# Kernel tuning notes

Hardware: AMD Instinct MI355X
Metric: run time of the kernel (lower is better)

Reference implementation:

```python
import jax, jax.numpy as jnp
import numpy as np

B, H, W, C = 4096, 64, 64, 8


def setup_inputs() -> dict:
    key = jax.random.key(0)
    k1, _ = jax.random.split(key)
    x = jax.random.randint(k1, (B, H, W, C), 0, 2).astype(jnp.float32)
    opp_start = jnp.array([3.0, 6.0], dtype=jnp.float32)
    return {"x": x, "opp_start": opp_start}


def reference(x, opp_start):
    Bb, Hh, Ww, _ = x.shape
    HW = Hh * Ww
    food = (x[..., 1] == 1.0)          # [B,H,W] bool
    opp = (x[..., 3] == 1.0)           # [B,H,W] bool
    food_f = food.reshape(Bb, HW)
    opp_f = opp.reshape(Bb, HW)
    n_food = food_f.sum(-1)
    n_opp = opp_f.sum(-1)

    # first opponent index in row-major order (torch.nonzero ordering)
    first_opp = jnp.argmax(opp_f, axis=-1)            # [B]
    orow = (first_opp // Ww).astype(jnp.float32)
    ocol = (first_opp % Ww).astype(jnp.float32)

    rows = jnp.arange(Hh, dtype=jnp.float32)[:, None]   # [H,1]
    cols = jnp.arange(Ww, dtype=jnp.float32)[None, :]   # [1,W]
    d = jnp.sqrt((rows - orow[:, None, None]) ** 2 + (cols - ocol[:, None, None]) ** 2)  # [B,H,W]
    INF = jnp.float32(np.inf)
    d = jnp.where(food, d, INF).reshape(Bb, HW)        # dists only at food cells

    min_idx = jnp.argmin(d, axis=-1)                   # first min, row-major (matches torch)
    min1 = jnp.take_along_axis(d, min_idx[:, None], axis=-1)[:, 0]
    d2 = d.at[jnp.arange(Bb), min_idx].set(INF)
    min2 = d2.min(-1)
    diff = min2 - min1                                 # sorted_dists[1]-sorted_dists[0]

    matches_start = (orow == opp_start[0]) & (ocol == opp_start[1])
    branchA = (n_food > 1) & (n_opp > 0) & (~matches_start)
    ambiguous = (branchA & (diff < 0.1)) | ((n_food > 1) & (~branchA))
    pick_nearest = (branchA & (diff >= 0.1)) | (n_food == 1)

    onehot_near = jax.nn.one_hot(min_idx, HW, dtype=jnp.float32)  # [B,HW]
    hit = jnp.where(ambiguous[:, None], food_f.astype(jnp.float32),
                    jnp.where(pick_nearest[:, None], onehot_near, 0.0))
    g_logits = -10.0 + 20.0 * hit
    return g_logits.reshape(Bb, Hh, Ww)
```

## Files before the change

### kernel.cpp

```cpp
#include <hip/hip_runtime.h>
#include <math.h>

constexpr int HWPIX = 4096;
constexpr int BLK   = 256;

__global__ __launch_bounds__(BLK) void oracle_kernel(
    const float* __restrict__ x,
    const float* __restrict__ opp_start,
    float* __restrict__ out)
{
    const int b    = blockIdx.x;
    const int t    = threadIdx.x;
    const int lane = t & 63;
    const int wv   = t >> 6;

    const float4* xb = (const float4*)(x + (size_t)b * HWPIX * 8);

    __shared__ unsigned char s_food[HWPIX];
    __shared__ int   s_stat[4][3];
    __shared__ float s_m1[4], s_m2[4];
    __shared__ int   s_i1[4];
    __shared__ int   s_hdr[3];
    __shared__ int   s_dec[3];

    const bool even  = (t & 1) == 0;
    const int  pbase = t >> 1;
    const int  j0    = b & 31;
    int fc = 0, oc = 0, fo = HWPIX;

    #pragma unroll
    for (int jo = 0; jo < 32; jo += 8) {
        float4 v[8];
        int    jj[8];
        #pragma unroll
        for (int ji = 0; ji < 8; ++ji) {
            jj[ji] = (j0 + jo + ji) & 31;
            v[ji]  = xb[t + BLK * jj[ji]];
        }
        #pragma unroll
        for (int ji = 0; ji < 8; ++ji) {
            const int  p    = pbase + 128 * jj[ji];
            const bool food = (v[ji].y == 1.0f);
            const bool opp  = (v[ji].w == 1.0f);
            if (even) {
                s_food[p] = food ? 1 : 0;
                fc += food ? 1 : 0;
                oc += opp  ? 1 : 0;
                fo  = opp ? min(fo, p) : fo;
            }
        }
    }

    #pragma unroll
    for (int off = 32; off > 0; off >>= 1) {
        fc += __shfl_down(fc, off);
        oc += __shfl_down(oc, off);
        fo  = min(fo, __shfl_down(fo, off));
    }
    if (lane == 0) { s_stat[wv][0] = fc; s_stat[wv][1] = oc; s_stat[wv][2] = fo; }
    __syncthreads();
    if (t == 0) {
        int nf = 0, no = 0, f = HWPIX;
        for (int w = 0; w < 4; ++w) {
            nf += s_stat[w][0]; no += s_stat[w][1]; f = min(f, s_stat[w][2]);
        }
        if (f == HWPIX) f = 0;
        s_hdr[0] = nf; s_hdr[1] = no; s_hdr[2] = f;
    }
    __syncthreads();
    const int n_food    = s_hdr[0];
    const int n_opp     = s_hdr[1];
    const int first_opp = s_hdr[2];
    const float orow = (float)(first_opp >> 6);
    const float ocol = (float)(first_opp & 63);

    float m1 = INFINITY, m2 = INFINITY;
    int   i1 = 0x7fffffff;
    #pragma unroll
    for (int k = 0; k < 16; ++k) {
        const int p = t + BLK * k;
        if (s_food[p]) {
            const float dr = (float)(p >> 6) - orow;
            const float dc = (float)(p & 63) - ocol;
            const float d  = sqrtf(dr * dr + dc * dc);
            if (d < m1)      { m2 = m1; m1 = d; i1 = p; }
            else if (d < m2) { m2 = d; }
        }
    }
    #pragma unroll
    for (int off = 32; off > 0; off >>= 1) {
        const float n1 = __shfl_down(m1, off);
        const int   j1 = __shfl_down(i1, off);
        const float n2 = __shfl_down(m2, off);
        if (n1 < m1 || (n1 == m1 && j1 < i1)) {
            m2 = fminf(m1, n2); m1 = n1; i1 = j1;
        } else {
            m2 = fminf(m2, n1);
        }
    }
    if (lane == 0) { s_m1[wv] = m1; s_m2[wv] = m2; s_i1[wv] = i1; }
    __syncthreads();

    if (t == 0) {
        m1 = s_m1[0]; m2 = s_m2[0]; i1 = s_i1[0];
        for (int w = 1; w < 4; ++w) {
            const float n1 = s_m1[w], n2 = s_m2[w];
            const int   j1 = s_i1[w];
            if (n1 < m1 || (n1 == m1 && j1 < i1)) {
                m2 = fminf(m1, n2); m1 = n1; i1 = j1;
            } else {
                m2 = fminf(m2, n1);
            }
        }
        const float diff = m2 - m1;
        const bool matches_start = (orow == opp_start[0]) && (ocol == opp_start[1]);
        const bool branchA   = (n_food > 1) && (n_opp > 0) && !matches_start;
        const bool ambiguous = (branchA && (diff < 0.1f)) || ((n_food > 1) && !branchA);
        const bool pick      = (branchA && (diff >= 0.1f)) || (n_food == 1);
        s_dec[0] = ambiguous ? 1 : 0;
        s_dec[1] = pick ? 1 : 0;
        s_dec[2] = i1;
    }
    __syncthreads();

    const int amb = s_dec[0], pick = s_dec[1], midx = s_dec[2];
    const unsigned* s_food32 = (const unsigned*)s_food;
    float4* ob4 = (float4*)(out + (size_t)b * HWPIX);
    #pragma unroll
    for (int k = 0; k < 4; ++k) {
        const int kk = (k + b) & 3;
        const int q = t + BLK * kk;
        const unsigned fm = s_food32[q];
        float4 r;
        float* rp = &r.x;
        #pragma unroll
        for (int i = 0; i < 4; ++i) {
            const int p = 4 * q + i;
            const bool f = (fm >> (8 * i)) & 0xFF;
            const float hit = amb ? (f ? 1.0f : 0.0f)
                                  : (pick ? ((p == midx) ? 1.0f : 0.0f) : 0.0f);
            rp[i] = -10.0f + 20.0f * hit;
        }
        ob4[q] = r;
    }
}

extern "C" void kernel_launch(void* const* d_in, const int* in_sizes, int n_in,
                              void* d_out, int out_size, void* d_ws, size_t ws_size,
                              hipStream_t stream) {
    const float* x         = (const float*)d_in[0];
    const float* opp_start = (const float*)d_in[1];
    float* out = (float*)d_out;
    const int B = in_sizes[0] / (HWPIX * 8);
    oracle_kernel<<<B, BLK, 0, stream>>>(x, opp_start, out);
}
```

Before: 697.0 us.

## Split input into streaming mask-compression pass and compact per-batch oracle kernel

Adds a grid-stride kernel that reads the float input once and writes a one-byte food/opponent mask per pixel into workspace. The oracle kernel then loads the compact mask with vector loads and computes counts and the first opponent with popcount and ctz. The aim is to decouple the bandwidth-heavy streaming from the reduction-heavy per-batch logic. In exchange it adds a kernel launch and an extra mask write and read through global memory.

```diff
diff --git a/kernel.cpp b/kernel.cpp
--- a/kernel.cpp
+++ b/kernel.cpp
@@ -1,11 +1,45 @@
 #include <hip/hip_runtime.h>
 #include <math.h>
 
-constexpr int HWPIX = 4096;
-constexpr int BLK   = 256;
+constexpr int HWPIX   = 4096;
+constexpr int BLK     = 256;
+constexpr int ABLOCKS = 2048;
+
+__global__ __launch_bounds__(BLK) void compress_kernel(
+    const float4* __restrict__ x4,
+    unsigned char* __restrict__ mask,
+    const long long n4)
+{
+    const long long NT = (long long)gridDim.x * BLK;
+    const bool even    = ((threadIdx.x & 1) == 0);
+    long long e = (long long)blockIdx.x * BLK + threadIdx.x;
+
+    for (; e + 7 * NT < n4; e += 8 * NT) {
+        float4 v[8];
+        #pragma unroll
+        for (int j = 0; j < 8; ++j)
+            v[j] = x4[e + (long long)j * NT];
+        if (even) {
+            #pragma unroll
+            for (int j = 0; j < 8; ++j) {
+                const long long ee = e + (long long)j * NT;
+                const unsigned char m =
+                    (unsigned char)((v[j].y == 1.0f ? 1u : 0u) |
+                                    (v[j].w == 1.0f ? 2u : 0u));
+                mask[ee >> 1] = m;
+            }
+        }
+    }
+    for (; e < n4; e += NT) {
+        const float4 v = x4[e];
+        if (even)
+            mask[e >> 1] = (unsigned char)((v.y == 1.0f ? 1u : 0u) |
+                                           (v.w == 1.0f ? 2u : 0u));
+    }
+}
 
 __global__ __launch_bounds__(BLK) void oracle_kernel(
-    const float* __restrict__ x,
+    const unsigned char* __restrict__ mask,
     const float* __restrict__ opp_start,
     float* __restrict__ out)
 {
@@ -14,8 +48,6 @@
     const int lane = t & 63;
     const int wv   = t >> 6;
 
-    const float4* xb = (const float4*)(x + (size_t)b * HWPIX * 8);
-
     __shared__ unsigned char s_food[HWPIX];
     __shared__ int   s_stat[4][3];
     __shared__ float s_m1[4], s_m2[4];
@@ -23,31 +55,25 @@
     __shared__ int   s_hdr[3];
     __shared__ int   s_dec[3];
 
-    const bool even  = (t & 1) == 0;
-    const int  pbase = t >> 1;
-    const int  j0    = b & 31;
+    const uint4* mb = (const uint4*)(mask + (size_t)b * HWPIX);
+    const uint4 w = mb[t];
+    unsigned md[4] = { w.x, w.y, w.z, w.w };
+    unsigned fd[4], od[4];
+    #pragma unroll
+    for (int j = 0; j < 4; ++j) {
+        fd[j] = md[j] & 0x01010101u;
+        od[j] = md[j] & 0x02020202u;
+    }
+    ((uint4*)s_food)[t] = make_uint4(fd[0], fd[1], fd[2], fd[3]);
+
     int fc = 0, oc = 0, fo = HWPIX;
-
     #pragma unroll
-    for (int jo = 0; jo < 32; jo += 8) {
-        float4 v[8];
-        int    jj[8];
-        #pragma unroll
-        for (int ji = 0; ji < 8; ++ji) {
-            jj[ji] = (j0 + jo + ji) & 31;
-            v[ji]  = xb[t + BLK * jj[ji]];
-        }
-        #pragma unroll
-        for (int ji = 0; ji < 8; ++ji) {
-            const int  p    = pbase + 128 * jj[ji];
-            const bool food = (v[ji].y == 1.0f);
-            const bool opp  = (v[ji].w == 1.0f);
-            if (even) {
-                s_food[p] = food ? 1 : 0;
-                fc += food ? 1 : 0;
-                oc += opp  ? 1 : 0;
-                fo  = opp ? min(fo, p) : fo;
-            }
+    for (int j = 0; j < 4; ++j) {
+        fc += __popc(fd[j]);
+        oc += __popc(od[j]);
+        if (od[j]) {
+            const int bidx = __builtin_ctz(od[j]) >> 3;
+            fo = min(fo, 16 * t + 4 * j + bidx);
         }
     }
 
@@ -61,8 +87,8 @@
     __syncthreads();
     if (t == 0) {
         int nf = 0, no = 0, f = HWPIX;
-        for (int w = 0; w < 4; ++w) {
-            nf += s_stat[w][0]; no += s_stat[w][1]; f = min(f, s_stat[w][2]);
+        for (int wq = 0; wq < 4; ++wq) {
+            nf += s_stat[wq][0]; no += s_stat[wq][1]; f = min(f, s_stat[wq][2]);
         }
         if (f == HWPIX) f = 0;
         s_hdr[0] = nf; s_hdr[1] = no; s_hdr[2] = f;
@@ -103,9 +129,9 @@
 
     if (t == 0) {
         m1 = s_m1[0]; m2 = s_m2[0]; i1 = s_i1[0];
-        for (int w = 1; w < 4; ++w) {
-            const float n1 = s_m1[w], n2 = s_m2[w];
-            const int   j1 = s_i1[w];
+        for (int wq = 1; wq < 4; ++wq) {
+            const float n1 = s_m1[wq], n2 = s_m2[wq];
+            const int   j1 = s_i1[wq];
             if (n1 < m1 || (n1 == m1 && j1 < i1)) {
                 m2 = fminf(m1, n2); m1 = n1; i1 = j1;
             } else {
@@ -152,5 +178,10 @@
     const float* opp_start = (const float*)d_in[1];
     float* out = (float*)d_out;
     const int B = in_sizes[0] / (HWPIX * 8);
-    oracle_kernel<<<B, BLK, 0, stream>>>(x, opp_start, out);
+
+    unsigned char* mask = (unsigned char*)d_ws;
+    const long long n4 = (long long)B * HWPIX * 2;
+
+    compress_kernel<<<ABLOCKS, BLK, 0, stream>>>((const float4*)x, mask, n4);
+    oracle_kernel<<<B, BLK, 0, stream>>>(mask, opp_start, out);
 }
```

After: 726.4 us. 1.04x slower.
